# Optimization experiments

Hardware: AMD Instinct MI355X
Metric: run time of the kernel (lower is better)

The kernel has to match this reference:

```python
import jax, jax.numpy as jnp
import numpy as np

B, N, D = 2, 2048, 768
HEADS, DIM_HEAD = 12, 64
INNER = HEADS * DIM_HEAD  # 768
OUT_DIM = 768


def setup_inputs() -> dict:
    key = jax.random.key(0)
    k1, k2, k3, k4, k5 = jax.random.split(key, 5)
    s_in = 1.0 / np.sqrt(D)
    s_inner = 1.0 / np.sqrt(INNER)
    return {
        "x": jax.random.normal(k1, (B, N, D), dtype=jnp.float32),
        "w_qkv": jax.random.normal(k2, (D, 3 * INNER), dtype=jnp.float32) * s_in,
        "b_qkv": jax.random.normal(k3, (3 * INNER,), dtype=jnp.float32) * 0.01,
        "w_out": jax.random.normal(k4, (INNER, OUT_DIM), dtype=jnp.float32) * s_inner,
        "b_out": jax.random.normal(k5, (OUT_DIM,), dtype=jnp.float32) * 0.01,
    }


def reference(x, w_qkv, b_qkv, w_out, b_out):
    b, n, _ = x.shape
    scale = DIM_HEAD ** -0.5
    qkv = x @ w_qkv + b_qkv                      # [b, n, 3*inner]
    q, k, v = jnp.split(qkv, 3, axis=-1)
    # 'b n (h d) -> b h n d'
    reshape = lambda t: t.reshape(b, n, HEADS, DIM_HEAD).transpose(0, 2, 1, 3)
    q, k, v = reshape(q), reshape(k), reshape(v)
    dots = jnp.einsum("bhnd,bhmd->bhnm", q, k) * scale
    attn = jax.nn.softmax(dots, axis=-1)
    out = jnp.einsum("bhnm,bhmd->bhnd", attn, v)  # [b, h, n, d]
    out = out.transpose(0, 2, 1, 3).reshape(b, n, INNER)
    return out @ w_out + b_out
```

## Files before the change

### kernel.cpp

```cpp
#include <hip/hip_runtime.h>
#include <hip/hip_bf16.h>
#include <stdint.h>


typedef __attribute__((ext_vector_type(8))) short bf16x8;
typedef __attribute__((ext_vector_type(4))) float f32x4;
typedef __attribute__((address_space(3))) unsigned int lds_uint;
typedef __attribute__((address_space(1))) const unsigned int g_uint;

__device__ __forceinline__ short f2bf(float f) {
    union { float f; uint32_t u; } x; x.f = f;
    uint32_t r = (x.u + 0x7fffu + ((x.u >> 16) & 1u)) >> 16;
    return (short)r;
}
__device__ __forceinline__ uint32_t packbf(float a, float b) {
    union { float f; uint32_t u; } xa, xb; xa.f = a; xb.f = b;
    return __builtin_amdgcn_perm(xb.u + 0x8000u, xa.u + 0x8000u, 0x07060302u);
}
__device__ __forceinline__ float exp2fast(float x) {
#if __has_builtin(__builtin_amdgcn_exp2f)
    return __builtin_amdgcn_exp2f(x);
#else
    return __expf(x * 0.6931471805599453f);
#endif
}
__device__ __forceinline__ void gl_lds16(const void* g, void* l) {
    __builtin_amdgcn_global_load_lds((g_uint*)g, (lds_uint*)l, 16, 0, 0);
}

__device__ __forceinline__ void tr_tile(const float* __restrict__ W,
                                        short* __restrict__ Wt, int K, int N,
                                        int n0, int k0, int t, short* S) {
    {
        int kl = t >> 2, ng = t & 3;
        const float* src = W + (size_t)(k0 + kl) * N + n0 + ng * 16;
        #pragma unroll
        for (int j = 0; j < 16; j += 4) {
            float4 f = *(const float4*)(src + j);
            S[(ng*16 + j + 0) * 65 + kl] = f2bf(f.x);
            S[(ng*16 + j + 1) * 65 + kl] = f2bf(f.y);
            S[(ng*16 + j + 2) * 65 + kl] = f2bf(f.z);
            S[(ng*16 + j + 3) * 65 + kl] = f2bf(f.w);
        }
    }
    __syncthreads();
    {
        int nl = t >> 2, kg = t & 3;
        short* dst = Wt + (size_t)(n0 + nl) * K + k0 + kg * 16;
        #pragma unroll
        for (int j = 0; j < 16; j += 4) {
            short4 s4;
            s4.x = S[nl*65 + kg*16 + j + 0];
            s4.y = S[nl*65 + kg*16 + j + 1];
            s4.z = S[nl*65 + kg*16 + j + 2];
            s4.w = S[nl*65 + kg*16 + j + 3];
            *(short4*)(dst + j) = s4;
        }
    }
}

__global__ __launch_bounds__(256)
void prep_k(const float* __restrict__ x, short* __restrict__ Xb,
            const float* __restrict__ Wq, short* __restrict__ Wqt,
            const float* __restrict__ Wo, short* __restrict__ Wot)
{
    __shared__ short S[64 * 65];
    const int t = threadIdx.x;
    if (blockIdx.x < 1536) {
        int i = (blockIdx.x * 256 + t) * 8;
        float4 f0 = *(const float4*)(x + i);
        float4 f1 = *(const float4*)(x + i + 4);
        short s[8];
        s[0]=f2bf(f0.x); s[1]=f2bf(f0.y); s[2]=f2bf(f0.z); s[3]=f2bf(f0.w);
        s[4]=f2bf(f1.x); s[5]=f2bf(f1.y); s[6]=f2bf(f1.z); s[7]=f2bf(f1.w);
        *(uint4*)(Xb + i) = *(uint4*)s;
        return;
    }
    if (blockIdx.x < 1968) {
        const int b2 = blockIdx.x - 1536;
        tr_tile(Wq, Wqt, 768, 2304, (b2 % 36) * 64, (b2 / 36) * 64, t, S);
    } else {
        const int b3 = blockIdx.x - 1968;
        tr_tile(Wo, Wot, 768, 768, (b3 % 12) * 64, (b3 / 12) * 64, t, S);
    }
}

__global__ __launch_bounds__(256)
void tr_w(const float* __restrict__ W, short* __restrict__ Wt, int K, int N) {
    __shared__ short S[64 * 65];
    tr_tile(W, Wt, K, N, blockIdx.x * 64, blockIdx.y * 64, threadIdx.x, S);
}

__global__ __launch_bounds__(256)
void gemm_qkv(const short* __restrict__ A, const short* __restrict__ Bt,
              const float* __restrict__ bias,
              short* __restrict__ Qb, short* __restrict__ Kb, short* __restrict__ Vt)
{
    __shared__ short As[2][128 * 32];
    __shared__ short Bs[2][96 * 32];
    const int tid = threadIdx.x, lane = tid & 63, w = tid >> 6;
    const int wm = w >> 1, wn = w & 1, quad = lane >> 4, lcol = lane & 15;
    const int bm = blockIdx.y * 128, bn = blockIdx.x * 96;

    f32x4 acc[4][3];
    #pragma unroll
    for (int i = 0; i < 4; i++)
        #pragma unroll
        for (int j = 0; j < 3; j++) acc[i][j] = (f32x4){0.f, 0.f, 0.f, 0.f};

    {
        #pragma unroll
        for (int i = 0; i < 2; i++) {
            int c = tid + i * 256, row = c >> 2, cs = c & 3;
            gl_lds16(A + (size_t)(bm + row) * 768 + cs * 8, As[0] + c * 8);
        }
        int c = tid, row = c >> 2, cs = c & 3;
        gl_lds16(Bt + (size_t)(bn + row) * 768 + cs * 8, Bs[0] + c * 8);
        if (tid < 128) {
            int c2 = 256 + tid, row2 = c2 >> 2, cs2 = c2 & 3;
            gl_lds16(Bt + (size_t)(bn + row2) * 768 + cs2 * 8, Bs[0] + c2 * 8);
        }
    }
    __syncthreads();

    for (int it = 0; it < 24; it++) {
        const int p = it & 1;
        if (it < 23) {
            int kt = (it + 1) * 32;
            #pragma unroll
            for (int i = 0; i < 2; i++) {
                int c = tid + i * 256, row = c >> 2, cs = c & 3;
                gl_lds16(A + (size_t)(bm + row) * 768 + kt + cs * 8, As[p ^ 1] + c * 8);
            }
            int c = tid, row = c >> 2, cs = c & 3;
            gl_lds16(Bt + (size_t)(bn + row) * 768 + kt + cs * 8, Bs[p ^ 1] + c * 8);
            if (tid < 128) {
                int c2 = 256 + tid, row2 = c2 >> 2, cs2 = c2 & 3;
                gl_lds16(Bt + (size_t)(bn + row2) * 768 + kt + cs2 * 8, Bs[p ^ 1] + c2 * 8);
            }
        }
        bf16x8 a[4], b[3];
        #pragma unroll
        for (int tm = 0; tm < 4; tm++)
            a[tm] = *(const bf16x8*)(As[p] + (wm*64 + tm*16 + lcol) * 32 + quad * 8);
        #pragma unroll
        for (int tn = 0; tn < 3; tn++)
            b[tn] = *(const bf16x8*)(Bs[p] + (wn*48 + tn*16 + lcol) * 32 + quad * 8);
        #pragma unroll
        for (int tm = 0; tm < 4; tm++)
            #pragma unroll
            for (int tn = 0; tn < 3; tn++)
                acc[tm][tn] = __builtin_amdgcn_mfma_f32_16x16x32_bf16(a[tm], b[tn], acc[tm][tn], 0, 0, 0);
        __syncthreads();
    }

    const float SCLQ = 0.18033688011112042f;
    #pragma unroll
    for (int tm = 0; tm < 4; tm++) {
        #pragma unroll
        for (int tn = 0; tn < 3; tn++) {
            int col = bn + wn*48 + tn*16 + lcol;
            float bv = bias[col];
            int which = (col >= 1536) ? 2 : (col >= 768 ? 1 : 0);
            int cc = col - which * 768;
            int h = cc >> 6, d = cc & 63;
            int rowbase = bm + wm*64 + tm*16 + quad*4;
            int bb = rowbase >> 11, n0 = rowbase & 2047;
            int bh = bb * 12 + h;
            if (which == 2) {
                short4 s4;
                s4.x = f2bf(acc[tm][tn][0] + bv);
                s4.y = f2bf(acc[tm][tn][1] + bv);
                s4.z = f2bf(acc[tm][tn][2] + bv);
                s4.w = f2bf(acc[tm][tn][3] + bv);
                *(short4*)(Vt + (((size_t)bh*32 + (n0 >> 6))*64 + d)*64 + (n0 & 63)) = s4;
            } else {
                #pragma unroll
                for (int reg = 0; reg < 4; reg++) {
                    float v = acc[tm][tn][reg] + bv;
                    if (which == 0) v *= SCLQ;
                    short* dst = (which == 0) ? Qb : Kb;
                    dst[((size_t)bh*2048 + n0 + reg)*64 + d] = f2bf(v);
                }
            }
        }
    }
}

__global__ __launch_bounds__(256)
void attn_k(const short* __restrict__ Q, const short* __restrict__ K,
            const short* __restrict__ Vt, short* __restrict__ Ab)
{
    __shared__ short Ks[2][4096];
    __shared__ short Vs[2][4096];

    const int tid = threadIdx.x, lane = tid & 63, w = tid >> 6;
    const int quad = lane >> 4, lcol = lane & 15;
    const int bid = blockIdx.x;
    const int bh = bid % 24, qt = bid / 24;
    const int b = bh / 12, h = bh - b * 12;

    const short* Kg = K  + (size_t)bh * 131072;
    const short* Vg = Vt + (size_t)bh * 131072;

    bf16x8 qf[2];
    {
        const short* Qg = Q + ((size_t)bh * 2048 + (size_t)qt * 64) * 64;
        #pragma unroll
        for (int ks = 0; ks < 2; ks++)
            qf[ks] = *(const bf16x8*)(Qg + (w*16 + lcol) * 64 + ks*32 + quad*8);
    }

    #pragma unroll
    for (int i = 0; i < 2; i++) {
        int c = tid + i * 256, row = c >> 3, cs = c & 7, gc = cs ^ (row & 7);
        gl_lds16(Kg + row * 64 + gc * 8, Ks[0] + c * 8);
        gl_lds16(Vg + row * 64 + gc * 8, Vs[0] + c * 8);
    }
    __syncthreads();

    f32x4 o[4];
    #pragma unroll
    for (int tn = 0; tn < 4; tn++) o[tn] = (f32x4){0.f, 0.f, 0.f, 0.f};
    float lp = 0.f;

    const int ksw = lcol & 7;
    const int bq  = ((quad & 1) << 1) | (quad >> 1);

    for (int kt = 0; kt < 32; kt++) {
        const int p = kt & 1;
        if (kt < 31) {
            #pragma unroll
            for (int i = 0; i < 2; i++) {
                int c = tid + i * 256, row = c >> 3, cs = c & 7, gc = cs ^ (row & 7);
                gl_lds16(Kg + (kt + 1) * 4096 + row * 64 + gc * 8, Ks[p ^ 1] + c * 8);
                gl_lds16(Vg + (kt + 1) * 4096 + row * 64 + gc * 8, Vs[p ^ 1] + c * 8);
            }
        }

        f32x4 st[4];
        #pragma unroll
        for (int kvs = 0; kvs < 4; kvs++) st[kvs] = (f32x4){0.f, 0.f, 0.f, 0.f};
        #pragma unroll
        for (int ks = 0; ks < 2; ks++) {
            #pragma unroll
            for (int kvs = 0; kvs < 4; kvs++) {
                bf16x8 kf = *(const bf16x8*)(Ks[p] + (kvs*16 + lcol) * 64 +
                                             (((ks*4 + quad) ^ ksw) << 3));
                st[kvs] = __builtin_amdgcn_mfma_f32_16x16x32_bf16(kf, qf[ks], st[kvs], 0, 0, 0);
            }
        }

        uint32_t X[4], Y[4];
        #pragma unroll
        for (int kvs = 0; kvs < 4; kvs++) {
            float p0 = exp2fast(st[kvs][0]), p1 = exp2fast(st[kvs][1]);
            float p2 = exp2fast(st[kvs][2]), p3 = exp2fast(st[kvs][3]);
            lp += (p0 + p1) + (p2 + p3);
            asm("v_cvt_pk_bf16_f32 %0, %1, %2" : "=v"(X[kvs]) : "v"(p0), "v"(p1));
            asm("v_cvt_pk_bf16_f32 %0, %1, %2" : "=v"(Y[kvs]) : "v"(p2), "v"(p3));
        }

        bf16x8 pa[2];
        #pragma unroll
        for (int ks = 0; ks < 2; ks++) {
            uint32_t a0 = X[2*ks], a1 = X[2*ks + 1];
            uint32_t b0 = Y[2*ks], b1 = Y[2*ks + 1];
            asm("v_permlane16_swap_b32 %0, %1" : "+v"(a0), "+v"(a1));
            asm("v_permlane16_swap_b32 %0, %1" : "+v"(b0), "+v"(b1));
            union { uint32_t u[4]; bf16x8 v; } pk_;
            pk_.u[0] = a0; pk_.u[1] = b0; pk_.u[2] = a1; pk_.u[3] = b1;
            pa[ks] = pk_.v;
        }

        #pragma unroll
        for (int ks = 0; ks < 2; ks++) {
            #pragma unroll
            for (int tn = 0; tn < 4; tn++) {
                int row = tn * 16 + lcol;
                bf16x8 bv = *(const bf16x8*)(Vs[p] + row * 64 +
                                             (((ks*4 + bq) ^ (row & 7)) << 3));
                o[tn] = __builtin_amdgcn_mfma_f32_16x16x32_bf16(pa[ks], bv, o[tn], 0, 0, 0);
            }
        }
        __syncthreads();
    }

    lp += __shfl_xor(lp, 16, 64);
    lp += __shfl_xor(lp, 32, 64);
    float rl[4];
    #pragma unroll
    for (int r = 0; r < 4; r++)
        rl[r] = 1.0f / __shfl(lp, quad * 4 + r, 64);

    #pragma unroll
    for (int tn = 0; tn < 4; tn++) {
        #pragma unroll
        for (int r = 0; r < 4; r++) {
            int q = qt * 64 + w * 16 + quad * 4 + r;
            int d = h * 64 + tn * 16 + lcol;
            Ab[((size_t)(b * 2048 + q)) * 768 + d] = f2bf(o[tn][r] * rl[r]);
        }
    }
}

__global__ __launch_bounds__(256)
void gemm_out(const short* __restrict__ A, const short* __restrict__ Bt,
              const float* __restrict__ bias, float* __restrict__ Of)
{
    __shared__ short As[2][64 * 32];
    __shared__ short Bs[2][96 * 32];
    const int tid = threadIdx.x, lane = tid & 63, w = tid >> 6;
    const int wm = w >> 1, wn = w & 1, quad = lane >> 4, lcol = lane & 15;
    const int bm = blockIdx.y * 64, bn = blockIdx.x * 96;

    f32x4 acc[2][3];
    #pragma unroll
    for (int i = 0; i < 2; i++)
        #pragma unroll
        for (int j = 0; j < 3; j++) acc[i][j] = (f32x4){0.f, 0.f, 0.f, 0.f};

    {
        int row = tid >> 2, cs = tid & 3;
        gl_lds16(A  + (size_t)(bm + row) * 768 + cs * 8, As[0] + tid * 8);
        gl_lds16(Bt + (size_t)(bn + row) * 768 + cs * 8, Bs[0] + tid * 8);
        if (tid < 128) {
            int c = 256 + tid, row2 = c >> 2, cs2 = c & 3;
            gl_lds16(Bt + (size_t)(bn + row2) * 768 + cs2 * 8, Bs[0] + c * 8);
        }
    }
    __syncthreads();

    for (int it = 0; it < 24; it++) {
        const int p = it & 1;
        if (it < 23) {
            int kt = (it + 1) * 32;
            int row = tid >> 2, cs = tid & 3;
            gl_lds16(A  + (size_t)(bm + row) * 768 + kt + cs * 8, As[p ^ 1] + tid * 8);
            gl_lds16(Bt + (size_t)(bn + row) * 768 + kt + cs * 8, Bs[p ^ 1] + tid * 8);
            if (tid < 128) {
                int c = 256 + tid, row2 = c >> 2, cs2 = c & 3;
                gl_lds16(Bt + (size_t)(bn + row2) * 768 + kt + cs2 * 8, Bs[p ^ 1] + c * 8);
            }
        }
        bf16x8 a[2], b[3];
        #pragma unroll
        for (int tm = 0; tm < 2; tm++)
            a[tm] = *(const bf16x8*)(As[p] + (wm*32 + tm*16 + lcol) * 32 + quad * 8);
        #pragma unroll
        for (int tn = 0; tn < 3; tn++)
            b[tn] = *(const bf16x8*)(Bs[p] + (wn*48 + tn*16 + lcol) * 32 + quad * 8);
        #pragma unroll
        for (int tm = 0; tm < 2; tm++)
            #pragma unroll
            for (int tn = 0; tn < 3; tn++)
                acc[tm][tn] = __builtin_amdgcn_mfma_f32_16x16x32_bf16(a[tm], b[tn], acc[tm][tn], 0, 0, 0);
        __syncthreads();
    }
    #pragma unroll
    for (int tm = 0; tm < 2; tm++) {
        #pragma unroll
        for (int tn = 0; tn < 3; tn++) {
            int col = bn + wn*48 + tn*16 + lcol;
            float bv = bias[col];
            #pragma unroll
            for (int reg = 0; reg < 4; reg++) {
                int row = bm + wm*32 + tm*16 + quad*4 + reg;
                Of[(size_t)row * 768 + col] = acc[tm][tn][reg] + bv;
            }
        }
    }
}

extern "C" void kernel_launch(void* const* d_in, const int* in_sizes, int n_in,
                              void* d_out, int out_size, void* d_ws, size_t ws_size,
                              hipStream_t stream)
{
    (void)in_sizes; (void)n_in; (void)out_size;
    const float* x     = (const float*)d_in[0];
    const float* w_qkv = (const float*)d_in[1];
    const float* b_qkv = (const float*)d_in[2];
    const float* w_out = (const float*)d_in[3];
    const float* b_out = (const float*)d_in[4];
    float* out = (float*)d_out;

    const size_t XSZ = (size_t)4096 * 768;
    const size_t WQ  = (size_t)2304 * 768;
    const size_t WO  = (size_t)768 * 768;
    const size_t HSZ = (size_t)24 * 2048 * 64;
    short* Xb  = (short*)d_ws;
    short* Wqt = Xb + XSZ;
    short* Qb  = Wqt + WQ;
    short* Kb  = Qb + HSZ;
    short* Vt  = Kb + HSZ;
    short* Ab  = Xb;

    const bool sepWot = ws_size >= (XSZ + WQ + 3*HSZ + WO) * sizeof(short);
    short* Wot = sepWot ? (Vt + HSZ) : Wqt;

    if (sepWot) {
        prep_k<<<2112, 256, 0, stream>>>(x, Xb, w_qkv, Wqt, w_out, Wot);
        gemm_qkv<<<dim3(24, 32), 256, 0, stream>>>(Xb, Wqt, b_qkv, Qb, Kb, Vt);
    } else {
        prep_k<<<1968, 256, 0, stream>>>(x, Xb, w_qkv, Wqt, w_out, Wot);
        gemm_qkv<<<dim3(24, 32), 256, 0, stream>>>(Xb, Wqt, b_qkv, Qb, Kb, Vt);
        tr_w<<<dim3(12, 12), 256, 0, stream>>>(w_out, Wot, 768, 768);
    }
    attn_k<<<768, 256, 0, stream>>>(Qb, Kb, Vt, Ab);
    gemm_out<<<dim3(8, 64), 256, 0, stream>>>(Ab, Wot, b_out, out);
}
```

Before: 156.4 us.

## Triple-buffer LDS tiles with explicit vmcnt waits in GEMM and attention kernels

Switches the QKV GEMM, attention and output GEMM kernels from double to triple LDS buffering, prefetching two tiles ahead. Each __syncthreads is replaced by a partial s_waitcnt vmcnt plus a raw barrier, so one stage of async global-to-LDS loads can stay in flight across the barrier. The goal is to hide global memory latency behind the MFMA work. In exchange it uses more LDS per block, which may lower occupancy. It also makes some threads issue redundant duplicate B-tile loads, added to keep the per-thread load count uniform for the vmcnt accounting.

New measurement: 161.3 us. +3.1%, slower.

```diff
diff --git a/kernel.cpp b/kernel.cpp
--- a/kernel.cpp
+++ b/kernel.cpp
@@ -12,10 +12,6 @@
     union { float f; uint32_t u; } x; x.f = f;
     uint32_t r = (x.u + 0x7fffu + ((x.u >> 16) & 1u)) >> 16;
     return (short)r;
-}
-__device__ __forceinline__ uint32_t packbf(float a, float b) {
-    union { float f; uint32_t u; } xa, xb; xa.f = a; xb.f = b;
-    return __builtin_amdgcn_perm(xb.u + 0x8000u, xa.u + 0x8000u, 0x07060302u);
 }
 __device__ __forceinline__ float exp2fast(float x) {
 #if __has_builtin(__builtin_amdgcn_exp2f)
@@ -27,6 +23,9 @@
 __device__ __forceinline__ void gl_lds16(const void* g, void* l) {
     __builtin_amdgcn_global_load_lds((g_uint*)g, (lds_uint*)l, 16, 0, 0);
 }
+#define WAITCNT_VM(N) asm volatile("s_waitcnt vmcnt(" #N ")" ::: "memory")
+#define BARRIER_FENCED() do { __builtin_amdgcn_s_barrier(); \
+                              asm volatile("" ::: "memory"); } while (0)
 
 __device__ __forceinline__ void tr_tile(const float* __restrict__ W,
                                         short* __restrict__ Wt, int K, int N,
@@ -96,8 +95,8 @@
               const float* __restrict__ bias,
               short* __restrict__ Qb, short* __restrict__ Kb, short* __restrict__ Vt)
 {
-    __shared__ short As[2][128 * 32];
-    __shared__ short Bs[2][96 * 32];
+    __shared__ short As[3][128 * 32];
+    __shared__ short Bs[3][96 * 32];
     const int tid = threadIdx.x, lane = tid & 63, w = tid >> 6;
     const int wm = w >> 1, wn = w & 1, quad = lane >> 4, lcol = lane & 15;
     const int bm = blockIdx.y * 128, bn = blockIdx.x * 96;
@@ -108,36 +107,31 @@
         #pragma unroll
         for (int j = 0; j < 3; j++) acc[i][j] = (f32x4){0.f, 0.f, 0.f, 0.f};
 
-    {
-        #pragma unroll
-        for (int i = 0; i < 2; i++) {
-            int c = tid + i * 256, row = c >> 2, cs = c & 3;
-            gl_lds16(A + (size_t)(bm + row) * 768 + cs * 8, As[0] + c * 8);
-        }
-        int c = tid, row = c >> 2, cs = c & 3;
-        gl_lds16(Bt + (size_t)(bn + row) * 768 + cs * 8, Bs[0] + c * 8);
-        if (tid < 128) {
-            int c2 = 256 + tid, row2 = c2 >> 2, cs2 = c2 & 3;
-            gl_lds16(Bt + (size_t)(bn + row2) * 768 + cs2 * 8, Bs[0] + c2 * 8);
-        }
-    }
-    __syncthreads();
+    const int ar0 = tid >> 2,          ac0 = (tid & 3) * 8;
+    const int ar1 = (tid + 256) >> 2,  ac1 = ac0;
+    const int br0 = tid >> 2,          bc0 = ac0;
+    const int c2  = 256 + (tid & 127);
+    const int br1 = c2 >> 2,           bc1 = (c2 & 3) * 8;
+
+    #pragma unroll
+    for (int t0 = 0; t0 < 2; t0++) {
+        const int kt = t0 * 32;
+        gl_lds16(A  + (size_t)(bm + ar0) * 768 + kt + ac0, As[t0] + tid * 8);
+        gl_lds16(A  + (size_t)(bm + ar1) * 768 + kt + ac1, As[t0] + (tid + 256) * 8);
+        gl_lds16(Bt + (size_t)(bn + br0) * 768 + kt + bc0, Bs[t0] + tid * 8);
+        gl_lds16(Bt + (size_t)(bn + br1) * 768 + kt + bc1, Bs[t0] + c2 * 8);
+    }
+    WAITCNT_VM(4);
+    BARRIER_FENCED();
 
     for (int it = 0; it < 24; it++) {
-        const int p = it & 1;
-        if (it < 23) {
-            int kt = (it + 1) * 32;
-            #pragma unroll
-            for (int i = 0; i < 2; i++) {
-                int c = tid + i * 256, row = c >> 2, cs = c & 3;
-                gl_lds16(A + (size_t)(bm + row) * 768 + kt + cs * 8, As[p ^ 1] + c * 8);
-            }
-            int c = tid, row = c >> 2, cs = c & 3;
-            gl_lds16(Bt + (size_t)(bn + row) * 768 + kt + cs * 8, Bs[p ^ 1] + c * 8);
-            if (tid < 128) {
-                int c2 = 256 + tid, row2 = c2 >> 2, cs2 = c2 & 3;
-                gl_lds16(Bt + (size_t)(bn + row2) * 768 + kt + cs2 * 8, Bs[p ^ 1] + c2 * 8);
-            }
+        const int p = it % 3;
+        if (it < 22) {
+            const int pb = (it + 2) % 3, kt = (it + 2) * 32;
+            gl_lds16(A  + (size_t)(bm + ar0) * 768 + kt + ac0, As[pb] + tid * 8);
+            gl_lds16(A  + (size_t)(bm + ar1) * 768 + kt + ac1, As[pb] + (tid + 256) * 8);
+            gl_lds16(Bt + (size_t)(bn + br0) * 768 + kt + bc0, Bs[pb] + tid * 8);
+            gl_lds16(Bt + (size_t)(bn + br1) * 768 + kt + bc1, Bs[pb] + c2 * 8);
         }
         bf16x8 a[4], b[3];
         #pragma unroll
@@ -151,7 +145,11 @@
             #pragma unroll
             for (int tn = 0; tn < 3; tn++)
                 acc[tm][tn] = __builtin_amdgcn_mfma_f32_16x16x32_bf16(a[tm], b[tn], acc[tm][tn], 0, 0, 0);
-        __syncthreads();
+        if (it < 23) {
+            if (it < 22) WAITCNT_VM(4);
+            else         WAITCNT_VM(0);
+            BARRIER_FENCED();
+        }
     }
 
     const float SCLQ = 0.18033688011112042f;
@@ -191,8 +189,8 @@
 void attn_k(const short* __restrict__ Q, const short* __restrict__ K,
             const short* __restrict__ Vt, short* __restrict__ Ab)
 {
-    __shared__ short Ks[2][4096];
-    __shared__ short Vs[2][4096];
+    __shared__ short Ks[3][4096];
+    __shared__ short Vs[3][4096];
 
     const int tid = threadIdx.x, lane = tid & 63, w = tid >> 6;
     const int quad = lane >> 4, lcol = lane & 15;
@@ -212,12 +210,16 @@
     }
 
     #pragma unroll
-    for (int i = 0; i < 2; i++) {
-        int c = tid + i * 256, row = c >> 3, cs = c & 7, gc = cs ^ (row & 7);
-        gl_lds16(Kg + row * 64 + gc * 8, Ks[0] + c * 8);
-        gl_lds16(Vg + row * 64 + gc * 8, Vs[0] + c * 8);
-    }
-    __syncthreads();
+    for (int t0 = 0; t0 < 2; t0++) {
+        #pragma unroll
+        for (int i = 0; i < 2; i++) {
+            int c = tid + i * 256, row = c >> 3, cs = c & 7, gc = cs ^ (row & 7);
+            gl_lds16(Kg + t0 * 4096 + row * 64 + gc * 8, Ks[t0] + c * 8);
+            gl_lds16(Vg + t0 * 4096 + row * 64 + gc * 8, Vs[t0] + c * 8);
+        }
+    }
+    WAITCNT_VM(4);
+    BARRIER_FENCED();
 
     f32x4 o[4];
     #pragma unroll
@@ -228,13 +230,16 @@
     const int bq  = ((quad & 1) << 1) | (quad >> 1);
 
     for (int kt = 0; kt < 32; kt++) {
-        const int p = kt & 1;
-        if (kt < 31) {
+        const int p = kt % 3;
+        if (kt < 30) {
+            const int pb = (kt + 2) % 3;
+            const short* Kn = Kg + (kt + 2) * 4096;
+            const short* Vn = Vg + (kt + 2) * 4096;
             #pragma unroll
             for (int i = 0; i < 2; i++) {
                 int c = tid + i * 256, row = c >> 3, cs = c & 7, gc = cs ^ (row & 7);
-                gl_lds16(Kg + (kt + 1) * 4096 + row * 64 + gc * 8, Ks[p ^ 1] + c * 8);
-                gl_lds16(Vg + (kt + 1) * 4096 + row * 64 + gc * 8, Vs[p ^ 1] + c * 8);
+                gl_lds16(Kn + row * 64 + gc * 8, Ks[pb] + c * 8);
+                gl_lds16(Vn + row * 64 + gc * 8, Vs[pb] + c * 8);
             }
         }
 
@@ -283,7 +288,12 @@
                 o[tn] = __builtin_amdgcn_mfma_f32_16x16x32_bf16(pa[ks], bv, o[tn], 0, 0, 0);
             }
         }
-        __syncthreads();
+
+        if (kt < 31) {
+            if (kt < 30) WAITCNT_VM(4);
+            else         WAITCNT_VM(0);
+            BARRIER_FENCED();
+        }
     }
 
     lp += __shfl_xor(lp, 16, 64);
@@ -308,8 +318,8 @@
 void gemm_out(const short* __restrict__ A, const short* __restrict__ Bt,
               const float* __restrict__ bias, float* __restrict__ Of)
 {
-    __shared__ short As[2][64 * 32];
-    __shared__ short Bs[2][96 * 32];
+    __shared__ short As[3][64 * 32];
+    __shared__ short Bs[3][96 * 32];
     const int tid = threadIdx.x, lane = tid & 63, w = tid >> 6;
     const int wm = w >> 1, wn = w & 1, quad = lane >> 4, lcol = lane & 15;
     const int bm = blockIdx.y * 64, bn = blockIdx.x * 96;
@@ -320,28 +330,27 @@
         #pragma unroll
         for (int j = 0; j < 3; j++) acc[i][j] = (f32x4){0.f, 0.f, 0.f, 0.f};
 
-    {
-        int row = tid >> 2, cs = tid & 3;
-        gl_lds16(A  + (size_t)(bm + row) * 768 + cs * 8, As[0] + tid * 8);
-        gl_lds16(Bt + (size_t)(bn + row) * 768 + cs * 8, Bs[0] + tid * 8);
-        if (tid < 128) {
-            int c = 256 + tid, row2 = c >> 2, cs2 = c & 3;
-            gl_lds16(Bt + (size_t)(bn + row2) * 768 + cs2 * 8, Bs[0] + c * 8);
-        }
-    }
-    __syncthreads();
+    const int ar0 = tid >> 2, ac0 = (tid & 3) * 8;
+    const int c2  = 256 + (tid & 127);
+    const int br1 = c2 >> 2,  bc1 = (c2 & 3) * 8;
+
+    #pragma unroll
+    for (int t0 = 0; t0 < 2; t0++) {
+        const int kt = t0 * 32;
+        gl_lds16(A  + (size_t)(bm + ar0) * 768 + kt + ac0, As[t0] + tid * 8);
+        gl_lds16(Bt + (size_t)(bn + ar0) * 768 + kt + ac0, Bs[t0] + tid * 8);
+        gl_lds16(Bt + (size_t)(bn + br1) * 768 + kt + bc1, Bs[t0] + c2 * 8);
+    }
+    WAITCNT_VM(3);
+    BARRIER_FENCED();
 
     for (int it = 0; it < 24; it++) {
-        const int p = it & 1;
-        if (it < 23) {
-            int kt = (it + 1) * 32;
-            int row = tid >> 2, cs = tid & 3;
-            gl_lds16(A  + (size_t)(bm + row) * 768 + kt + cs * 8, As[p ^ 1] + tid * 8);
-            gl_lds16(Bt + (size_t)(bn + row) * 768 + kt + cs * 8, Bs[p ^ 1] + tid * 8);
-            if (tid < 128) {
-                int c = 256 + tid, row2 = c >> 2, cs2 = c & 3;
-                gl_lds16(Bt + (size_t)(bn + row2) * 768 + kt + cs2 * 8, Bs[p ^ 1] + c * 8);
-            }
+        const int p = it % 3;
+        if (it < 22) {
+            const int pb = (it + 2) % 3, kt = (it + 2) * 32;
+            gl_lds16(A  + (size_t)(bm + ar0) * 768 + kt + ac0, As[pb] + tid * 8);
+            gl_lds16(Bt + (size_t)(bn + ar0) * 768 + kt + ac0, Bs[pb] + tid * 8);
+            gl_lds16(Bt + (size_t)(bn + br1) * 768 + kt + bc1, Bs[pb] + c2 * 8);
         }
         bf16x8 a[2], b[3];
         #pragma unroll
@@ -355,7 +364,11 @@
             #pragma unroll
             for (int tn = 0; tn < 3; tn++)
                 acc[tm][tn] = __builtin_amdgcn_mfma_f32_16x16x32_bf16(a[tm], b[tn], acc[tm][tn], 0, 0, 0);
-        __syncthreads();
+        if (it < 23) {
+            if (it < 22) WAITCNT_VM(3);
+            else         WAITCNT_VM(0);
+            BARRIER_FENCED();
+        }
     }
     #pragma unroll
     for (int tm = 0; tm < 2; tm++) {
```

## Triple-buffer attention K/V tiles and split warps 2x2 over query and key halves

Applied to the files above, without the earlier changes.

The attention kernel moves from double to triple buffering of K/V tiles, prefetching two tiles ahead. It replaces __syncthreads with explicit vmcnt waits and raw barriers. Warps are regrouped 2x2: each covers 32 query rows and half of the key dimension of a tile, so each K fragment load feeds two MFMAs and each V fragment load feeds two. Partial outputs and row sums from the key halves are then reduced through LDS at the end. This adds LDS use, an extra reduction step and more reliance on hand-written wait counts in exchange for less LDS traffic per MFMA and deeper load overlap.

New measurement: 164.8 us. 1.05x slower.

```diff
diff --git a/kernel.cpp b/kernel.cpp
--- a/kernel.cpp
+++ b/kernel.cpp
@@ -12,10 +12,6 @@
     union { float f; uint32_t u; } x; x.f = f;
     uint32_t r = (x.u + 0x7fffu + ((x.u >> 16) & 1u)) >> 16;
     return (short)r;
-}
-__device__ __forceinline__ uint32_t packbf(float a, float b) {
-    union { float f; uint32_t u; } xa, xb; xa.f = a; xb.f = b;
-    return __builtin_amdgcn_perm(xb.u + 0x8000u, xa.u + 0x8000u, 0x07060302u);
 }
 __device__ __forceinline__ float exp2fast(float x) {
 #if __has_builtin(__builtin_amdgcn_exp2f)
@@ -27,6 +23,9 @@
 __device__ __forceinline__ void gl_lds16(const void* g, void* l) {
     __builtin_amdgcn_global_load_lds((g_uint*)g, (lds_uint*)l, 16, 0, 0);
 }
+#define WAITCNT_VM(N) asm volatile("s_waitcnt vmcnt(" #N ")" ::: "memory")
+#define BARRIER_FENCED() do { __builtin_amdgcn_s_barrier(); \
+                              asm volatile("" ::: "memory"); } while (0)
 
 __device__ __forceinline__ void tr_tile(const float* __restrict__ W,
                                         short* __restrict__ Wt, int K, int N,
@@ -191,11 +190,12 @@
 void attn_k(const short* __restrict__ Q, const short* __restrict__ K,
             const short* __restrict__ Vt, short* __restrict__ Ab)
 {
-    __shared__ short Ks[2][4096];
-    __shared__ short Vs[2][4096];
+    __shared__ __align__(16) short Ks[3][4096];
+    __shared__ __align__(16) short Vs[3][4096];
 
     const int tid = threadIdx.x, lane = tid & 63, w = tid >> 6;
     const int quad = lane >> 4, lcol = lane & 15;
+    const int qh = w >> 1, kh = w & 1;
     const int bid = blockIdx.x;
     const int bh = bid % 24, qt = bid / 24;
     const int b = bh / 12, h = bh - b * 12;
@@ -203,103 +203,155 @@
     const short* Kg = K  + (size_t)bh * 131072;
     const short* Vg = Vt + (size_t)bh * 131072;
 
-    bf16x8 qf[2];
+    bf16x8 qf[2][2];
     {
-        const short* Qg = Q + ((size_t)bh * 2048 + (size_t)qt * 64) * 64;
-        #pragma unroll
-        for (int ks = 0; ks < 2; ks++)
-            qf[ks] = *(const bf16x8*)(Qg + (w*16 + lcol) * 64 + ks*32 + quad*8);
-    }
-
-    #pragma unroll
-    for (int i = 0; i < 2; i++) {
-        int c = tid + i * 256, row = c >> 3, cs = c & 7, gc = cs ^ (row & 7);
-        gl_lds16(Kg + row * 64 + gc * 8, Ks[0] + c * 8);
-        gl_lds16(Vg + row * 64 + gc * 8, Vs[0] + c * 8);
-    }
-    __syncthreads();
-
-    f32x4 o[4];
-    #pragma unroll
-    for (int tn = 0; tn < 4; tn++) o[tn] = (f32x4){0.f, 0.f, 0.f, 0.f};
-    float lp = 0.f;
+        const short* Qg = Q + ((size_t)bh * 2048 + (size_t)qt * 64 + qh * 32) * 64;
+        #pragma unroll
+        for (int qs = 0; qs < 2; qs++)
+            #pragma unroll
+            for (int ks = 0; ks < 2; ks++)
+                qf[qs][ks] = *(const bf16x8*)(Qg + (qs*16 + lcol) * 64 + ks*32 + quad*8);
+    }
+
+    #pragma unroll
+    for (int t0 = 0; t0 < 2; t0++) {
+        #pragma unroll
+        for (int i = 0; i < 2; i++) {
+            int c = tid + i * 256, row = c >> 3, cs = c & 7, gc = cs ^ (row & 7);
+            gl_lds16(Kg + t0 * 4096 + row * 64 + gc * 8, Ks[t0] + c * 8);
+            gl_lds16(Vg + t0 * 4096 + row * 64 + gc * 8, Vs[t0] + c * 8);
+        }
+    }
+    WAITCNT_VM(4);
+    BARRIER_FENCED();
+
+    f32x4 o[2][4];
+    #pragma unroll
+    for (int qs = 0; qs < 2; qs++)
+        #pragma unroll
+        for (int tn = 0; tn < 4; tn++) o[qs][tn] = (f32x4){0.f, 0.f, 0.f, 0.f};
+    float lp[2] = {0.f, 0.f};
 
     const int ksw = lcol & 7;
     const int bq  = ((quad & 1) << 1) | (quad >> 1);
 
     for (int kt = 0; kt < 32; kt++) {
-        const int p = kt & 1;
-        if (kt < 31) {
+        const int p = kt % 3;
+        if (kt < 30) {
+            const int pb = (kt + 2) % 3;
+            const short* Kn = Kg + (kt + 2) * 4096;
+            const short* Vn = Vg + (kt + 2) * 4096;
             #pragma unroll
             for (int i = 0; i < 2; i++) {
                 int c = tid + i * 256, row = c >> 3, cs = c & 7, gc = cs ^ (row & 7);
-                gl_lds16(Kg + (kt + 1) * 4096 + row * 64 + gc * 8, Ks[p ^ 1] + c * 8);
-                gl_lds16(Vg + (kt + 1) * 4096 + row * 64 + gc * 8, Vs[p ^ 1] + c * 8);
-            }
-        }
-
-        f32x4 st[4];
-        #pragma unroll
-        for (int kvs = 0; kvs < 4; kvs++) st[kvs] = (f32x4){0.f, 0.f, 0.f, 0.f};
+                gl_lds16(Kn + row * 64 + gc * 8, Ks[pb] + c * 8);
+                gl_lds16(Vn + row * 64 + gc * 8, Vs[pb] + c * 8);
+            }
+        }
+
+        f32x4 st[2][2];
+        #pragma unroll
+        for (int kvs = 0; kvs < 2; kvs++)
+            #pragma unroll
+            for (int qs = 0; qs < 2; qs++) st[kvs][qs] = (f32x4){0.f, 0.f, 0.f, 0.f};
         #pragma unroll
         for (int ks = 0; ks < 2; ks++) {
             #pragma unroll
-            for (int kvs = 0; kvs < 4; kvs++) {
-                bf16x8 kf = *(const bf16x8*)(Ks[p] + (kvs*16 + lcol) * 64 +
+            for (int kvs = 0; kvs < 2; kvs++) {
+                bf16x8 kf = *(const bf16x8*)(Ks[p] + (kh*32 + kvs*16 + lcol) * 64 +
                                              (((ks*4 + quad) ^ ksw) << 3));
-                st[kvs] = __builtin_amdgcn_mfma_f32_16x16x32_bf16(kf, qf[ks], st[kvs], 0, 0, 0);
-            }
-        }
-
-        uint32_t X[4], Y[4];
-        #pragma unroll
-        for (int kvs = 0; kvs < 4; kvs++) {
-            float p0 = exp2fast(st[kvs][0]), p1 = exp2fast(st[kvs][1]);
-            float p2 = exp2fast(st[kvs][2]), p3 = exp2fast(st[kvs][3]);
-            lp += (p0 + p1) + (p2 + p3);
-            asm("v_cvt_pk_bf16_f32 %0, %1, %2" : "=v"(X[kvs]) : "v"(p0), "v"(p1));
-            asm("v_cvt_pk_bf16_f32 %0, %1, %2" : "=v"(Y[kvs]) : "v"(p2), "v"(p3));
+                #pragma unroll
+                for (int qs = 0; qs < 2; qs++)
+                    st[kvs][qs] = __builtin_amdgcn_mfma_f32_16x16x32_bf16(kf, qf[qs][ks], st[kvs][qs], 0, 0, 0);
+            }
+        }
+
+        uint32_t X[2][2], Y[2][2];
+        #pragma unroll
+        for (int kvs = 0; kvs < 2; kvs++) {
+            #pragma unroll
+            for (int qs = 0; qs < 2; qs++) {
+                float p0 = exp2fast(st[kvs][qs][0]), p1 = exp2fast(st[kvs][qs][1]);
+                float p2 = exp2fast(st[kvs][qs][2]), p3 = exp2fast(st[kvs][qs][3]);
+                lp[qs] += (p0 + p1) + (p2 + p3);
+                asm("v_cvt_pk_bf16_f32 %0, %1, %2" : "=v"(X[kvs][qs]) : "v"(p0), "v"(p1));
+                asm("v_cvt_pk_bf16_f32 %0, %1, %2" : "=v"(Y[kvs][qs]) : "v"(p2), "v"(p3));
+            }
         }
 
         bf16x8 pa[2];
         #pragma unroll
-        for (int ks = 0; ks < 2; ks++) {
-            uint32_t a0 = X[2*ks], a1 = X[2*ks + 1];
-            uint32_t b0 = Y[2*ks], b1 = Y[2*ks + 1];
+        for (int qs = 0; qs < 2; qs++) {
+            uint32_t a0 = X[0][qs], a1 = X[1][qs];
+            uint32_t b0 = Y[0][qs], b1 = Y[1][qs];
             asm("v_permlane16_swap_b32 %0, %1" : "+v"(a0), "+v"(a1));
             asm("v_permlane16_swap_b32 %0, %1" : "+v"(b0), "+v"(b1));
             union { uint32_t u[4]; bf16x8 v; } pk_;
             pk_.u[0] = a0; pk_.u[1] = b0; pk_.u[2] = a1; pk_.u[3] = b1;
-            pa[ks] = pk_.v;
-        }
-
-        #pragma unroll
-        for (int ks = 0; ks < 2; ks++) {
+            pa[qs] = pk_.v;
+        }
+
+        #pragma unroll
+        for (int tn = 0; tn < 4; tn++) {
+            int row = tn * 16 + lcol;
+            bf16x8 bv = *(const bf16x8*)(Vs[p] + row * 64 +
+                                         (((kh*4 + bq) ^ (row & 7)) << 3));
+            #pragma unroll
+            for (int qs = 0; qs < 2; qs++)
+                o[qs][tn] = __builtin_amdgcn_mfma_f32_16x16x32_bf16(pa[qs], bv, o[qs][tn], 0, 0, 0);
+        }
+
+        if (kt < 31) {
+            if (kt < 30) WAITCNT_VM(4);
+            else         WAITCNT_VM(0);
+            BARRIER_FENCED();
+        }
+    }
+
+    #pragma unroll
+    for (int qs = 0; qs < 2; qs++) {
+        lp[qs] += __shfl_xor(lp[qs], 16, 64);
+        lp[qs] += __shfl_xor(lp[qs], 32, 64);
+    }
+
+    float* scr = (float*)&Ks[0][0];
+    const int obase = qh * 2304;
+    __syncthreads();
+    if (kh) {
+        #pragma unroll
+        for (int qs = 0; qs < 2; qs++)
+            #pragma unroll
+            for (int tn = 0; tn < 4; tn++)
+                *(f32x4*)(scr + obase + ((qs*4 + tn) * 64 + lane) * 4) = o[qs][tn];
+        scr[obase + 2048 + lane*2 + 0] = lp[0];
+        scr[obase + 2048 + lane*2 + 1] = lp[1];
+    }
+    __syncthreads();
+    if (!kh) {
+        #pragma unroll
+        for (int qs = 0; qs < 2; qs++) {
             #pragma unroll
             for (int tn = 0; tn < 4; tn++) {
-                int row = tn * 16 + lcol;
-                bf16x8 bv = *(const bf16x8*)(Vs[p] + row * 64 +
-                                             (((ks*4 + bq) ^ (row & 7)) << 3));
-                o[tn] = __builtin_amdgcn_mfma_f32_16x16x32_bf16(pa[ks], bv, o[tn], 0, 0, 0);
-            }
-        }
-        __syncthreads();
-    }
-
-    lp += __shfl_xor(lp, 16, 64);
-    lp += __shfl_xor(lp, 32, 64);
-    float rl[4];
-    #pragma unroll
-    for (int r = 0; r < 4; r++)
-        rl[r] = 1.0f / __shfl(lp, quad * 4 + r, 64);
-
-    #pragma unroll
-    for (int tn = 0; tn < 4; tn++) {
-        #pragma unroll
-        for (int r = 0; r < 4; r++) {
-            int q = qt * 64 + w * 16 + quad * 4 + r;
-            int d = h * 64 + tn * 16 + lcol;
-            Ab[((size_t)(b * 2048 + q)) * 768 + d] = f2bf(o[tn][r] * rl[r]);
+                f32x4 t = *(const f32x4*)(scr + obase + ((qs*4 + tn) * 64 + lane) * 4);
+                o[qs][tn] += t;
+            }
+            lp[qs] += scr[obase + 2048 + lane*2 + qs];
+        }
+        #pragma unroll
+        for (int qs = 0; qs < 2; qs++) {
+            float rl[4];
+            #pragma unroll
+            for (int r = 0; r < 4; r++)
+                rl[r] = 1.0f / __shfl(lp[qs], quad * 4 + r, 64);
+            #pragma unroll
+            for (int tn = 0; tn < 4; tn++) {
+                #pragma unroll
+                for (int r = 0; r < 4; r++) {
+                    int q = qt * 64 + qh * 32 + qs * 16 + quad * 4 + r;
+                    int d = h * 64 + tn * 16 + lcol;
+                    Ab[((size_t)(b * 2048 + q)) * 768 + d] = f2bf(o[qs][tn][r] * rl[r]);
+                }
+            }
         }
     }
 }
```
